# Kernel optimization log

Hardware: AMD Instinct MI355X
Metric: run time of the kernel (lower is better)

The kernel has to match this reference:

```python
import jax, jax.numpy as jnp
import numpy as np
import math

D = 1024
H = 16
HD = D // H  # 64
SCALE = math.sqrt(HD)


def setup_inputs() -> dict:
    key = jax.random.key(0)
    ks = jax.random.split(key, 4)
    B, S = 2, 2048
    x = jax.random.normal(ks[0], (B, S, D), dtype=jnp.float32)
    attention_mask = jnp.zeros((B, S), dtype=jnp.float32)  # additive mask
    w_attn = jax.random.normal(ks[1], (D, 3 * D), dtype=jnp.float32) * (1.0 / math.sqrt(D))
    b_attn = jnp.zeros((3 * D,), dtype=jnp.float32)
    w_proj = jax.random.normal(ks[2], (D, D), dtype=jnp.float32) * (1.0 / math.sqrt(D))
    b_proj = jnp.zeros((D,), dtype=jnp.float32)
    return {"x": x, "attention_mask": attention_mask, "w_attn": w_attn,
            "b_attn": b_attn, "w_proj": w_proj, "b_proj": b_proj}


def reference(x, attention_mask, w_attn, b_attn, w_proj, b_proj):
    B, S, _ = x.shape
    qkv = x @ w_attn + b_attn                      # [B,S,3D]
    q, k, v = jnp.split(qkv, 3, axis=-1)           # each [B,S,D]
    # split heads -> [B,H,S,HD]
    sh = lambda t: t.reshape(B, S, H, HD).transpose(0, 2, 1, 3)
    q, k, v = sh(q), sh(k), sh(v)
    scores = jnp.einsum('bhqd,bhkd->bhqk', q, k) / SCALE   # [B,H,S,S]
    scores = scores + attention_mask[:, None, None, :]      # additive mask [B,1,1,S]
    attn = jax.nn.softmax(scores, axis=-1)                  # dropout disabled (eval)
    out = jnp.einsum('bhqk,bhkd->bhqd', attn, v)            # [B,H,S,HD]
    out = out.transpose(0, 2, 1, 3).reshape(B, S, D)        # merge heads
    out = out @ w_proj + b_proj                              # resid dropout disabled
    return out
```

## Files before the change

kernel.cpp:

```cpp
#include <hip/hip_runtime.h>
#include <math.h>

#define B_  2
#define S_  2048
#define D_  1024
#define H_  16
#define HD_ 64
#define BS_ (B_ * S_)

#define LOG2E_   1.44269504088896f
#define CSCALE_  (0.125f * LOG2E_)

typedef float f32x4 __attribute__((ext_vector_type(4)));
typedef int   i32x4 __attribute__((ext_vector_type(4)));

__device__ __forceinline__ float bf2f(unsigned short u) {
    union { unsigned int i; float f; } c; c.i = ((unsigned int)u) << 16; return c.f;
}
__device__ __forceinline__ unsigned short f2bf(float f) {
    union { float f; unsigned int i; } c; c.f = f;
    unsigned int r = c.i + 0x7FFFu + ((c.i >> 16) & 1u);
    return (unsigned short)(r >> 16);
}
__device__ __forceinline__ unsigned int cvtpk_bf16(float lo, float hi) {
    unsigned int r;
    asm volatile("v_cvt_pk_bf16_f32 %0, %1, %2" : "=v"(r) : "v"(lo), "v"(hi));
    return r;
}
__device__ __forceinline__ void gl_lds16(const void* g, void* l) {
    __builtin_amdgcn_global_load_lds((const __attribute__((address_space(1))) void*)g,
                                     (__attribute__((address_space(3))) void*)l, 16, 0, 0);
}
__device__ __forceinline__ void mfma_bf16(f32x4& d, i32x4 a, i32x4 b) {
    asm volatile("v_mfma_f32_16x16x32_bf16 %0, %1, %2, %0" : "+v"(d) : "v"(a), "v"(b));
}

__global__ __launch_bounds__(256) void convert_f32_bf16(
    const float* __restrict__ in, unsigned short* __restrict__ out, int n)
{
    const int i = (blockIdx.x * 256 + threadIdx.x) * 8;
    if (i >= n) return;
    const float4 a = *reinterpret_cast<const float4*>(in + i);
    const float4 b = *reinterpret_cast<const float4*>(in + i + 4);
    ushort4 u0 = make_ushort4(f2bf(a.x), f2bf(a.y), f2bf(a.z), f2bf(a.w));
    ushort4 u1 = make_ushort4(f2bf(b.x), f2bf(b.y), f2bf(b.z), f2bf(b.w));
    *reinterpret_cast<ushort4*>(out + i)     = u0;
    *reinterpret_cast<ushort4*>(out + i + 4) = u1;
}

__global__ __launch_bounds__(256) void scale_mask(
    const float* __restrict__ m, float* __restrict__ m2, int n)
{
    const int i = blockIdx.x * 256 + threadIdx.x;
    if (i < n) m2[i] = m[i] * LOG2E_;
}

__global__ __launch_bounds__(256) void transpose_cvt(
    const float* __restrict__ W, unsigned short* __restrict__ Wt, int K, int N)
{
    __shared__ float t[32][33];
    const int n0 = blockIdx.x * 32, k0 = blockIdx.y * 32;
    const int tx = threadIdx.x & 31, ty = threadIdx.x >> 5;
#pragma unroll
    for (int r = 0; r < 32; r += 8)
        t[ty + r][tx] = W[(size_t)(k0 + ty + r) * N + n0 + tx];
    __syncthreads();
#pragma unroll
    for (int r = 0; r < 32; r += 8)
        Wt[(size_t)(n0 + ty + r) * K + k0 + tx] = f2bf(t[tx][ty + r]);
}

template <typename OutT, int BN>
__global__ __launch_bounds__(256) void gemm_bt_bf16(
    const unsigned short* __restrict__ A,
    const unsigned short* __restrict__ Bt,
    const float* __restrict__ bias,
    OutT* __restrict__ C, int M, int N, int K)
{
    constexpr int NW = BN / 2;
    constexpr int NI = NW / 16;
    __shared__ alignas(16) unsigned short As[2][4096];
    __shared__ alignas(16) unsigned short Bs[2][BN * 32];

    const int tid  = threadIdx.x;
    const int wave = tid >> 6;
    const int l    = tid & 63;
    const int g    = l >> 4;
    const int r    = l & 15;
    const int wr   = wave >> 1, wc = wave & 1;
    const int row0 = blockIdx.y * 128;
    const int col0 = blockIdx.x * BN;

    const size_t aoff0 = (size_t)(row0 +   0 + l) * K + wave * 8;
    const size_t aoff1 = (size_t)(row0 +  64 + l) * K + wave * 8;
    const size_t boff0 = (size_t)(col0 +   0 + l) * K + wave * 8;
    const size_t boff1 = (size_t)(col0 +  64 + l) * K + wave * 8;

    auto stage = [&](int kt, int buf) {
        gl_lds16(A + aoff0 + kt, &As[buf][wave * 1024]);
        gl_lds16(A + aoff1 + kt, &As[buf][wave * 1024 + 512]);
        if constexpr (BN == 128) {
            gl_lds16(Bt + boff0 + kt, &Bs[buf][wave * 1024]);
            gl_lds16(Bt + boff1 + kt, &Bs[buf][wave * 1024 + 512]);
        } else {
            gl_lds16(Bt + boff0 + kt, &Bs[buf][wave * 512]);
        }
    };

    f32x4 acc[4][NI];
#pragma unroll
    for (int mi = 0; mi < 4; ++mi)
#pragma unroll
        for (int ni = 0; ni < NI; ++ni) acc[mi][ni] = (f32x4)0.f;

    stage(0, 0);
    __syncthreads();

    for (int kt = 0; kt < K; kt += 32) {
        const int cur = (kt >> 5) & 1;
        if (kt + 32 < K) stage(kt + 32, cur ^ 1);

        const unsigned short* Ab = &As[cur][g * 1024];
        const unsigned short* Bb = &Bs[cur][g * (BN * 8)];
        i32x4 af[4], bf[NI];
#pragma unroll
        for (int mi = 0; mi < 4; ++mi)
            af[mi] = *reinterpret_cast<const i32x4*>(Ab + (wr * 64 + mi * 16 + r) * 8);
#pragma unroll
        for (int ni = 0; ni < NI; ++ni)
            bf[ni] = *reinterpret_cast<const i32x4*>(Bb + (wc * NW + ni * 16 + r) * 8);
#pragma unroll
        for (int mi = 0; mi < 4; ++mi)
#pragma unroll
            for (int ni = 0; ni < NI; ++ni)
                mfma_bf16(acc[mi][ni], af[mi], bf[ni]);

        __syncthreads();
    }

#pragma unroll
    for (int ni = 0; ni < NI; ++ni) {
        const int n = col0 + wc * NW + ni * 16 + r;
        const float bv = bias[n];
#pragma unroll
        for (int mi = 0; mi < 4; ++mi) {
#pragma unroll
            for (int e = 0; e < 4; ++e) {
                const int m = row0 + wr * 64 + mi * 16 + g * 4 + e;
                const float val = acc[mi][ni][e] + bv;
                if constexpr (sizeof(OutT) == 2)
                    C[(size_t)m * N + n] = (OutT)f2bf(val);
                else
                    C[(size_t)m * N + n] = (OutT)val;
            }
        }
    }
}

__global__ __launch_bounds__(512) void flash_attn_mfma(
    const unsigned short* __restrict__ qkv,
    const float* __restrict__ mask2,
    unsigned short* __restrict__ out)
{
    __shared__ alignas(16) unsigned short Klds[2][4096];
    __shared__ alignas(16) unsigned short Vt[2][4096];

    const int tid  = threadIdx.x;
    const int wave = tid >> 6;
    const int l    = tid & 63;
    const int g    = l >> 4;
    const int r    = l & 15;
    const int b    = blockIdx.z;
    const int h    = blockIdx.y;
    const int q0   = blockIdx.x * 128;
    const int qw   = q0 + wave * 16;

    const size_t rs = 3 * (size_t)D_;
    const unsigned short* qb = qkv + (size_t)b * S_ * rs + (size_t)h * HD_;
    const unsigned short* kb = qb + D_;
    const unsigned short* vb = qb + 2 * D_;
    const float* m2row = mask2 + (size_t)b * S_;

    i32x4 qf[2];
#pragma unroll
    for (int ks = 0; ks < 2; ++ks)
        qf[ks] = *reinterpret_cast<const i32x4*>(
            qb + (size_t)(qw + r) * rs + ks * 32 + g * 8);

    const int kkey = (wave & 3) * 16 + (l >> 3);
    const int kuni = ((l & 7) ^ (l >> 3)) * 8;
    const int vkey = (wave & 3) * 16 + (l >> 2);
    const int vpart = l & 3;

    auto stage = [&](int kt, int buf) {
        if (wave < 4) {
            gl_lds16(kb + (size_t)(kt + kkey) * rs + kuni,
                     &Klds[buf][(wave & 3) * 1024]);
            gl_lds16(kb + (size_t)(kt + kkey + 8) * rs + kuni,
                     &Klds[buf][(wave & 3) * 1024 + 512]);
        } else {
#pragma unroll
            for (int p = 0; p < 4; ++p) {
                const int d0 = p * 16 + vpart * 4;
                const ushort4 vv = *reinterpret_cast<const ushort4*>(
                    vb + (size_t)(kt + vkey) * rs + d0);
                Vt[buf][(d0 + 0) * 64 + (vkey ^ (((d0 + 0) & 7) << 3))] = vv.x;
                Vt[buf][(d0 + 1) * 64 + (vkey ^ (((d0 + 1) & 7) << 3))] = vv.y;
                Vt[buf][(d0 + 2) * 64 + (vkey ^ (((d0 + 2) & 7) << 3))] = vv.z;
                Vt[buf][(d0 + 3) * 64 + (vkey ^ (((d0 + 3) & 7) << 3))] = vv.w;
            }
        }
    };

    f32x4 acc[4];
    float m_i = -1e30f, l_i = 0.f;
#pragma unroll
    for (int mi = 0; mi < 4; ++mi) acc[mi] = (f32x4)0.f;

    stage(0, 0);
    __syncthreads();

    for (int kt = 0; kt < S_; kt += 64) {
        const int cur = (kt >> 6) & 1;
        if (kt + 64 < S_) stage(kt + 64, cur ^ 1);

        const unsigned short* Kb = Klds[cur];
        const unsigned short* Vb = Vt[cur];

        f32x4 s[4];
#pragma unroll
        for (int mi = 0; mi < 4; ++mi) s[mi] = (f32x4)0.f;
        __builtin_amdgcn_s_setprio(1);
#pragma unroll
        for (int ks = 0; ks < 2; ++ks)
#pragma unroll
            for (int mi = 0; mi < 4; ++mi) {
                const i32x4 kf = *reinterpret_cast<const i32x4*>(
                    Kb + (mi * 16 + r) * 64 + ((ks * 32 + g * 8) ^ ((r & 7) << 3)));
                mfma_bf16(s[mi], kf, qf[ks]);
            }
        __builtin_amdgcn_s_setprio(0);

#pragma unroll
        for (int mi = 0; mi < 4; ++mi) {
            const float4 mk = *reinterpret_cast<const float4*>(
                m2row + kt + mi * 16 + g * 4);
            s[mi][0] = s[mi][0] * CSCALE_ + mk.x;
            s[mi][1] = s[mi][1] * CSCALE_ + mk.y;
            s[mi][2] = s[mi][2] * CSCALE_ + mk.z;
            s[mi][3] = s[mi][3] * CSCALE_ + mk.w;
        }

        float tmax = -1e30f;
#pragma unroll
        for (int mi = 0; mi < 4; ++mi)
#pragma unroll
            for (int e = 0; e < 4; ++e)
                tmax = fmaxf(tmax, s[mi][e]);
        tmax = fmaxf(tmax, __shfl_xor(tmax, 16));
        tmax = fmaxf(tmax, __shfl_xor(tmax, 32));
        if (tmax > m_i + 4.f) {
            const float corr = exp2f(m_i - tmax);
            l_i *= corr;
#pragma unroll
            for (int mi = 0; mi < 4; ++mi) acc[mi] *= corr;
            m_i = tmax;
        }

        unsigned int pk[4][2];
        float ls = 0.f;
#pragma unroll
        for (int mi = 0; mi < 4; ++mi) {
            const float p0 = exp2f(s[mi][0] - m_i);
            const float p1 = exp2f(s[mi][1] - m_i);
            const float p2 = exp2f(s[mi][2] - m_i);
            const float p3 = exp2f(s[mi][3] - m_i);
            ls += (p0 + p1) + (p2 + p3);
            pk[mi][0] = cvtpk_bf16(p0, p1);
            pk[mi][1] = cvtpk_bf16(p2, p3);
        }
        l_i += ls;

#pragma unroll
        for (int ks = 0; ks < 2; ++ks) {
            i32x4 pf;
#pragma unroll
            for (int w = 0; w < 4; ++w) {
                const int src = (((g & 1) * 2 + (w >> 1)) << 4) + r;
                const unsigned int vA = __shfl(pk[2 * ks + 0][w & 1], src);
                const unsigned int vB = __shfl(pk[2 * ks + 1][w & 1], src);
                pf[w] = (int)((g >> 1) ? vB : vA);
            }
            __builtin_amdgcn_s_setprio(1);
#pragma unroll
            for (int mi = 0; mi < 4; ++mi) {
                const i32x4 vf = *reinterpret_cast<const i32x4*>(
                    Vb + (mi * 16 + r) * 64 + ((ks * 32 + g * 8) ^ ((r & 7) << 3)));
                mfma_bf16(acc[mi], vf, pf);
            }
            __builtin_amdgcn_s_setprio(0);
        }

        __syncthreads();
    }

    float lf = l_i;
    lf += __shfl_xor(lf, 16);
    lf += __shfl_xor(lf, 32);
    const float inv = 1.0f / lf;
    const size_t token = (size_t)b * S_ + qw + r;
#pragma unroll
    for (int mi = 0; mi < 4; ++mi) {
        const f32x4 v = acc[mi] * inv;
        uint2 w;
        w.x = cvtpk_bf16(v[0], v[1]);
        w.y = cvtpk_bf16(v[2], v[3]);
        *reinterpret_cast<uint2*>(
            out + token * D_ + h * HD_ + mi * 16 + g * 4) = w;
    }
}

extern "C" void kernel_launch(void* const* d_in, const int* in_sizes, int n_in,
                              void* d_out, int out_size, void* d_ws, size_t ws_size,
                              hipStream_t stream)
{
    const float* x      = (const float*)d_in[0];
    const float* amask  = (const float*)d_in[1];
    const float* w_attn = (const float*)d_in[2];
    const float* b_attn = (const float*)d_in[3];
    const float* w_proj = (const float*)d_in[4];
    const float* b_proj = (const float*)d_in[5];
    float* out = (float*)d_out;

    unsigned short* qkvb  = (unsigned short*)d_ws;
    unsigned short* attnb = qkvb  + (size_t)BS_ * 3 * D_;
    unsigned short* xb    = attnb + (size_t)BS_ * D_;
    unsigned short* wat   = xb    + (size_t)BS_ * D_;
    unsigned short* wpt   = wat   + (size_t)3 * D_ * D_;
    float*          mask2 = (float*)(wpt + (size_t)D_ * D_);

    convert_f32_bf16<<<(BS_ * D_) / 2048, 256, 0, stream>>>(x, xb, BS_ * D_);
    scale_mask<<<BS_ / 256, 256, 0, stream>>>(amask, mask2, BS_);
    transpose_cvt<<<dim3(3 * D_ / 32, D_ / 32), 256, 0, stream>>>(w_attn, wat, D_, 3 * D_);
    transpose_cvt<<<dim3(D_ / 32, D_ / 32), 256, 0, stream>>>(w_proj, wpt, D_, D_);

    gemm_bt_bf16<unsigned short, 128><<<dim3(3 * D_ / 128, BS_ / 128), 256, 0, stream>>>(
        xb, wat, b_attn, qkvb, BS_, 3 * D_, D_);

    flash_attn_mfma<<<dim3(S_ / 128, H_, B_), 512, 0, stream>>>(qkvb, mask2, attnb);

    gemm_bt_bf16<float, 128><<<dim3(D_ / 128, BS_ / 128), 256, 0, stream>>>(
        attnb, wpt, b_proj, out, BS_, D_, D_);
}
```

Before: 186.5 us.

## Split attention KV range across two blocks and merge with a combine kernel

Splits the key/value sequence into two halves, launching twice as many attention blocks (a split-KV flash-decoding scheme) so more blocks are in flight across CUs. Each half writes normalized bf16 partial outputs plus per-row max and sum, and a new combine kernel rescales and merges them into the final attention buffer, reusing dead workspace (xb, wat) as scratch. It also drops the setprio hints around the MFMA sections. The cost is an extra kernel launch, extra global traffic for partial outputs, and a second bf16 rounding of the partials.

```diff
diff --git a/kernel.cpp b/kernel.cpp
--- a/kernel.cpp
+++ b/kernel.cpp
@@ -7,6 +7,7 @@
 #define H_  16
 #define HD_ 64
 #define BS_ (B_ * S_)
+#define SH_ (S_ / 2)
 
 #define LOG2E_   1.44269504088896f
 #define CSCALE_  (0.125f * LOG2E_)
@@ -157,10 +158,12 @@
     }
 }
 
-__global__ __launch_bounds__(512) void flash_attn_mfma(
+__global__ __launch_bounds__(512) void flash_attn_split(
     const unsigned short* __restrict__ qkv,
     const float* __restrict__ mask2,
-    unsigned short* __restrict__ out)
+    unsigned short* __restrict__ op0,
+    unsigned short* __restrict__ op1,
+    float2* __restrict__ ml)
 {
     __shared__ alignas(16) unsigned short Klds[2][4096];
     __shared__ alignas(16) unsigned short Vt[2][4096];
@@ -170,7 +173,10 @@
     const int l    = tid & 63;
     const int g    = l >> 4;
     const int r    = l & 15;
-    const int b    = blockIdx.z;
+    const int z    = blockIdx.z;
+    const int b    = z >> 1;
+    const int half = z & 1;
+    const int kv0  = half * SH_;
     const int h    = blockIdx.y;
     const int q0   = blockIdx.x * 128;
     const int qw   = q0 + wave * 16;
@@ -217,12 +223,12 @@
 #pragma unroll
     for (int mi = 0; mi < 4; ++mi) acc[mi] = (f32x4)0.f;
 
-    stage(0, 0);
+    stage(kv0, 0);
     __syncthreads();
 
-    for (int kt = 0; kt < S_; kt += 64) {
-        const int cur = (kt >> 6) & 1;
-        if (kt + 64 < S_) stage(kt + 64, cur ^ 1);
+    for (int kt = kv0; kt < kv0 + SH_; kt += 64) {
+        const int cur = ((kt - kv0) >> 6) & 1;
+        if (kt + 64 < kv0 + SH_) stage(kt + 64, cur ^ 1);
 
         const unsigned short* Kb = Klds[cur];
         const unsigned short* Vb = Vt[cur];
@@ -230,7 +236,6 @@
         f32x4 s[4];
 #pragma unroll
         for (int mi = 0; mi < 4; ++mi) s[mi] = (f32x4)0.f;
-        __builtin_amdgcn_s_setprio(1);
 #pragma unroll
         for (int ks = 0; ks < 2; ++ks)
 #pragma unroll
@@ -239,7 +244,6 @@
                     Kb + (mi * 16 + r) * 64 + ((ks * 32 + g * 8) ^ ((r & 7) << 3)));
                 mfma_bf16(s[mi], kf, qf[ks]);
             }
-        __builtin_amdgcn_s_setprio(0);
 
 #pragma unroll
         for (int mi = 0; mi < 4; ++mi) {
@@ -291,14 +295,12 @@
                 const unsigned int vB = __shfl(pk[2 * ks + 1][w & 1], src);
                 pf[w] = (int)((g >> 1) ? vB : vA);
             }
-            __builtin_amdgcn_s_setprio(1);
 #pragma unroll
             for (int mi = 0; mi < 4; ++mi) {
                 const i32x4 vf = *reinterpret_cast<const i32x4*>(
                     Vb + (mi * 16 + r) * 64 + ((ks * 32 + g * 8) ^ ((r & 7) << 3)));
                 mfma_bf16(acc[mi], vf, pf);
             }
-            __builtin_amdgcn_s_setprio(0);
         }
 
         __syncthreads();
@@ -309,6 +311,7 @@
     lf += __shfl_xor(lf, 32);
     const float inv = 1.0f / lf;
     const size_t token = (size_t)b * S_ + qw + r;
+    unsigned short* obase = half ? op1 : op0;
 #pragma unroll
     for (int mi = 0; mi < 4; ++mi) {
         const f32x4 v = acc[mi] * inv;
@@ -316,8 +319,51 @@
         w.x = cvtpk_bf16(v[0], v[1]);
         w.y = cvtpk_bf16(v[2], v[3]);
         *reinterpret_cast<uint2*>(
-            out + token * D_ + h * HD_ + mi * 16 + g * 4) = w;
+            obase + token * D_ + h * HD_ + mi * 16 + g * 4) = w;
     }
+    if (l < 16) {
+        const size_t mli = (((size_t)half * B_ + b) * H_ + h) * S_ + qw + l;
+        ml[mli] = make_float2(m_i, lf);
+    }
+}
+
+__global__ __launch_bounds__(256) void combine_halves(
+    unsigned short* o0,
+    const unsigned short* __restrict__ o1,
+    const float2* __restrict__ ml)
+{
+    const int gid   = blockIdx.x * 256 + threadIdx.x;
+    const int chunk = gid & 127;
+    const int token = gid >> 7;
+    const int h     = chunk >> 3;
+    const int b     = token >> 11;
+    const int q     = token & 2047;
+
+    const size_t mli = (((size_t)b) * H_ + h) * S_ + q;
+    const float2 a0 = ml[mli];
+    const float2 a1 = ml[(size_t)B_ * H_ * S_ + mli];
+    const float M  = fmaxf(a0.x, a1.x);
+    float w0 = a0.y * exp2f(a0.x - M);
+    float w1 = a1.y * exp2f(a1.x - M);
+    const float inv = 1.0f / (w0 + w1);
+    w0 *= inv; w1 *= inv;
+
+    const size_t off = (size_t)token * D_ + chunk * 8;
+    const ushort4 x0 = *reinterpret_cast<const ushort4*>(o0 + off);
+    const ushort4 x1 = *reinterpret_cast<const ushort4*>(o0 + off + 4);
+    const ushort4 y0 = *reinterpret_cast<const ushort4*>(o1 + off);
+    const ushort4 y1 = *reinterpret_cast<const ushort4*>(o1 + off + 4);
+    ushort4 r0, r1;
+    r0.x = f2bf(w0 * bf2f(x0.x) + w1 * bf2f(y0.x));
+    r0.y = f2bf(w0 * bf2f(x0.y) + w1 * bf2f(y0.y));
+    r0.z = f2bf(w0 * bf2f(x0.z) + w1 * bf2f(y0.z));
+    r0.w = f2bf(w0 * bf2f(x0.w) + w1 * bf2f(y0.w));
+    r1.x = f2bf(w0 * bf2f(x1.x) + w1 * bf2f(y1.x));
+    r1.y = f2bf(w0 * bf2f(x1.y) + w1 * bf2f(y1.y));
+    r1.z = f2bf(w0 * bf2f(x1.z) + w1 * bf2f(y1.z));
+    r1.w = f2bf(w0 * bf2f(x1.w) + w1 * bf2f(y1.w));
+    *reinterpret_cast<ushort4*>(o0 + off)     = r0;
+    *reinterpret_cast<ushort4*>(o0 + off + 4) = r1;
 }
 
 extern "C" void kernel_launch(void* const* d_in, const int* in_sizes, int n_in,
@@ -338,6 +384,7 @@
     unsigned short* wat   = xb    + (size_t)BS_ * D_;
     unsigned short* wpt   = wat   + (size_t)3 * D_ * D_;
     float*          mask2 = (float*)(wpt + (size_t)D_ * D_);
+    float2*         mlbuf = (float2*)wat;
 
     convert_f32_bf16<<<(BS_ * D_) / 2048, 256, 0, stream>>>(x, xb, BS_ * D_);
     scale_mask<<<BS_ / 256, 256, 0, stream>>>(amask, mask2, BS_);
@@ -347,7 +394,10 @@
     gemm_bt_bf16<unsigned short, 128><<<dim3(3 * D_ / 128, BS_ / 128), 256, 0, stream>>>(
         xb, wat, b_attn, qkvb, BS_, 3 * D_, D_);
 
-    flash_attn_mfma<<<dim3(S_ / 128, H_, B_), 512, 0, stream>>>(qkvb, mask2, attnb);
+    flash_attn_split<<<dim3(S_ / 128, H_, B_ * 2), 512, 0, stream>>>(
+        qkvb, mask2, attnb, xb, mlbuf);
+
+    combine_halves<<<(BS_ * D_ / 8) / 256, 256, 0, stream>>>(attnb, xb, mlbuf);
 
     gemm_bt_bf16<float, 128><<<dim3(D_ / 128, BS_ / 128), 256, 0, stream>>>(
         attnb, wpt, b_proj, out, BS_, D_, D_);
```

Result: slower. 196.7 us (+5.4%).
